# Kernel tuning notes

Measured on AMD Instinct MI355X. Metric: run time of the kernel, lower is better.

## Reference

```python
import jax, jax.numpy as jnp
import numpy as np

N_NODES = 50000
N_EDGES = 800000
IN_FEATS = 256
H_FEATS = 256
NUM_CLASSES = 128


def setup_inputs() -> dict:
    key = jax.random.key(0)
    ks = jax.random.split(key, 5)
    x = jax.random.normal(ks[0], (N_NODES, IN_FEATS), dtype=jnp.float32)
    src = jax.random.randint(ks[1], (N_EDGES,), 0, N_NODES, dtype=jnp.int64)
    dst = jax.random.randint(ks[2], (N_EDGES,), 0, N_NODES, dtype=jnp.int64)
    W1 = jax.random.normal(ks[3], (IN_FEATS, H_FEATS), dtype=jnp.float32) * (1.0 / np.sqrt(IN_FEATS))
    b1 = jnp.zeros((H_FEATS,), dtype=jnp.float32)
    W2 = jax.random.normal(ks[4], (H_FEATS, NUM_CLASSES), dtype=jnp.float32) * (1.0 / np.sqrt(H_FEATS))
    b2 = jnp.zeros((NUM_CLASSES,), dtype=jnp.float32)
    return {"x": x, "src": src, "dst": dst, "W1": W1, "b1": b1, "W2": W2, "b2": b2}


def _graph_conv(x, src, dst, norm_src, norm_dst, W, b):
    # DGL GraphConv, norm='both': D_out^{-1/2} A D_in^{-1/2} X W + b
    # project first (in_feats >= out_feats -> cheaper messages), math identical
    h = (x * norm_src[:, None]) @ W                      # [N, out]
    agg = jax.ops.segment_sum(h[src], dst, num_segments=N_NODES)  # gather + scatter-add
    return agg * norm_dst[:, None] + b


def reference(x, src, dst, W1, b1, W2, b2):
    ones = jnp.ones((N_EDGES,), dtype=x.dtype)
    deg_out = jax.ops.segment_sum(ones, src, num_segments=N_NODES)
    deg_in = jax.ops.segment_sum(ones, dst, num_segments=N_NODES)
    norm_src = jnp.clip(deg_out, 1.0, None) ** -0.5
    norm_dst = jnp.clip(deg_in, 1.0, None) ** -0.5

    h = _graph_conv(x, src, dst, norm_src, norm_dst, W1, b1)
    h = jax.nn.relu(h)
    out = _graph_conv(h, src, dst, norm_src, norm_dst, W2, b2)
    return out
```

## Files before the change

### kernel.cpp

```cpp
#include <hip/hip_runtime.h>

#define NNODES 50000
#define MPAD   50048
#define NEDGES 800000
#define KDIM   256
#define FH     256
#define FOUT   128

#define SHIFT  8
#define NBUCK  196
#define NB1    200
#define EPB    4000
#define CELLS  (NBUCK * NB1)
#define NSCAN  (2 * CELLS)
#define SCANB  ((NSCAN + 511) / 512)

typedef __bf16 bf16x8 __attribute__((ext_vector_type(8)));
typedef float floatx4 __attribute__((ext_vector_type(4)));

__device__ __forceinline__ float bf2f(unsigned short u) {
    union { unsigned int i; float f; } v;
    v.i = ((unsigned int)u) << 16;
    return v.f;
}
__device__ __forceinline__ unsigned short f2bf(float f) {
    union { float f; unsigned int i; } v;
    v.f = f;
    unsigned int r = v.i + 0x7FFFu + ((v.i >> 16) & 1u);
    return (unsigned short)(r >> 16);
}

__global__ __launch_bounds__(256) void l1_count_cast(const int* __restrict__ src,
                                                     const int* __restrict__ dst,
                                                     int* __restrict__ cell,
                                                     const float* __restrict__ W1,
                                                     unsigned short* __restrict__ Wt1,
                                                     const float* __restrict__ W2,
                                                     unsigned short* __restrict__ Wt2) {
    __shared__ int histD[256], histS[256];
    __shared__ float tile[32][33];
    const int tid = threadIdx.x;

    if (blockIdx.x >= NB1) {
        int b = blockIdx.x - NB1;
        const float* W; unsigned short* Wt; int N;
        if (b < 64) { W = W1; Wt = Wt1; N = FH; }
        else        { b -= 64; W = W2; Wt = Wt2; N = FOUT; }
        int kt = (b & 7) * 32;
        int nt = (b >> 3) * 32;
        int tx = tid & 31;
        int ty = tid >> 5;
        for (int r = ty; r < 32; r += 8)
            tile[r][tx] = W[(size_t)(kt + r) * N + nt + tx];
        __syncthreads();
        for (int r = ty; r < 32; r += 8)
            Wt[(size_t)(nt + r) * KDIM + kt + tx] = f2bf(tile[tx][r]);
        return;
    }

    const int b = blockIdx.x;
    const int base = b * EPB;
    histD[tid] = 0; histS[tid] = 0;
    __syncthreads();
    for (int g = tid; g < EPB / 4; g += 256) {
        uint4 s4 = *(const uint4*)(src + base + g * 4);
        uint4 d4 = *(const uint4*)(dst + base + g * 4);
        atomicAdd(&histD[d4.x >> SHIFT], 1);
        atomicAdd(&histD[d4.y >> SHIFT], 1);
        atomicAdd(&histD[d4.z >> SHIFT], 1);
        atomicAdd(&histD[d4.w >> SHIFT], 1);
        atomicAdd(&histS[s4.x >> SHIFT], 1);
        atomicAdd(&histS[s4.y >> SHIFT], 1);
        atomicAdd(&histS[s4.z >> SHIFT], 1);
        atomicAdd(&histS[s4.w >> SHIFT], 1);
    }
    __syncthreads();
    if (tid < NBUCK) {
        cell[tid * NB1 + b] = histD[tid];
        cell[CELLS + tid * NB1 + b] = histS[tid];
    }
}

__global__ __launch_bounds__(512) void scanA(int* __restrict__ data,
                                             int* __restrict__ sums, int n) {
    __shared__ int s[512];
    int tid = threadIdx.x;
    int i = blockIdx.x * 512 + tid;
    int v = (i < n) ? data[i] : 0;
    s[tid] = v;
    __syncthreads();
    for (int off = 1; off < 512; off <<= 1) {
        int t = (tid >= off) ? s[tid - off] : 0;
        __syncthreads();
        s[tid] += t;
        __syncthreads();
    }
    if (i < n) data[i] = s[tid] - v;
    if (tid == 511) sums[blockIdx.x] = s[511];
}

__global__ __launch_bounds__(512) void scanB(int* __restrict__ sums, int nb) {
    __shared__ int s[512];
    int tid = threadIdx.x;
    int v = (tid < nb) ? sums[tid] : 0;
    s[tid] = v;
    __syncthreads();
    for (int off = 1; off < 512; off <<= 1) {
        int t = (tid >= off) ? s[tid - off] : 0;
        __syncthreads();
        s[tid] += t;
        __syncthreads();
    }
    if (tid < nb) sums[tid] = s[tid] - v;
}

__global__ __launch_bounds__(512) void scanC(int* __restrict__ data,
                                             const int* __restrict__ sums, int n) {
    int i = blockIdx.x * 512 + threadIdx.x;
    if (i < n) data[i] += sums[blockIdx.x];
}

__global__ __launch_bounds__(256) void l1_scatter(const int* __restrict__ src,
                                                  const int* __restrict__ dst,
                                                  const int* __restrict__ cell,
                                                  unsigned int* __restrict__ tmp1,
                                                  unsigned char* __restrict__ tmp2) {
    __shared__ int histD[256], histS[256];
    __shared__ int exD[256], exS[256];
    __shared__ unsigned int bufD[EPB];
    __shared__ unsigned short bufS[EPB];
    const int b = blockIdx.x, tid = threadIdx.x;
    const int base = b * EPB;

    histD[tid] = 0; histS[tid] = 0;
    __syncthreads();
    for (int g = tid; g < EPB / 4; g += 256) {
        uint4 s4 = *(const uint4*)(src + base + g * 4);
        uint4 d4 = *(const uint4*)(dst + base + g * 4);
        atomicAdd(&histD[d4.x >> SHIFT], 1);
        atomicAdd(&histD[d4.y >> SHIFT], 1);
        atomicAdd(&histD[d4.z >> SHIFT], 1);
        atomicAdd(&histD[d4.w >> SHIFT], 1);
        atomicAdd(&histS[s4.x >> SHIFT], 1);
        atomicAdd(&histS[s4.y >> SHIFT], 1);
        atomicAdd(&histS[s4.z >> SHIFT], 1);
        atomicAdd(&histS[s4.w >> SHIFT], 1);
    }
    __syncthreads();
    int vD = histD[tid], vS = histS[tid];
    exD[tid] = vD; exS[tid] = vS;
    __syncthreads();
    for (int off = 1; off < 256; off <<= 1) {
        int tD = (tid >= off) ? exD[tid - off] : 0;
        int tS = (tid >= off) ? exS[tid - off] : 0;
        __syncthreads();
        exD[tid] += tD; exS[tid] += tS;
        __syncthreads();
    }
    int eD = exD[tid] - vD, eS = exS[tid] - vS;
    __syncthreads();
    exD[tid] = eD; exS[tid] = eS;
    histD[tid] = eD; histS[tid] = eS;
    __syncthreads();
    for (int g = tid; g < EPB / 4; g += 256) {
        uint4 s4 = *(const uint4*)(src + base + g * 4);
        uint4 d4 = *(const uint4*)(dst + base + g * 4);
        unsigned int ss[4] = {s4.x, s4.y, s4.z, s4.w};
        unsigned int dd[4] = {d4.x, d4.y, d4.z, d4.w};
#pragma unroll
        for (int j = 0; j < 4; ++j) {
            int p = atomicAdd(&histD[dd[j] >> SHIFT], 1);
            bufD[p] = (ss[j] << 16) | dd[j];
            int q = atomicAdd(&histS[ss[j] >> SHIFT], 1);
            bufS[q] = (unsigned short)ss[j];
        }
    }
    __syncthreads();
    for (int e = tid; e < EPB; e += 256) {
        unsigned int p = bufD[e];
        int k = (p & 0xFFFFu) >> SHIFT;
        tmp1[cell[k * NB1 + b] + (e - exD[k])] = p;
    }
    for (int e = tid; e < EPB; e += 256) {
        unsigned int s = bufS[e];
        int k = s >> SHIFT;
        tmp2[(cell[CELLS + k * NB1 + b] - NEDGES) + (e - exS[k])] = (unsigned char)(s & 255u);
    }
}

__global__ __launch_bounds__(256) void l2_both(const unsigned int* __restrict__ tmp1,
                                               const unsigned char* __restrict__ tmp2,
                                               const int* __restrict__ cell,
                                               int* __restrict__ row_ptr,
                                               float* __restrict__ norm_dst,
                                               float* __restrict__ norm_src,
                                               int* __restrict__ csr_src) {
    __shared__ int cnt[256], ofs[256], cur[256];
    const int tid = threadIdx.x;

    if (blockIdx.x >= NBUCK) {
        const int k = blockIdx.x - NBUCK;
        const int start = cell[CELLS + k * NB1] - NEDGES;
        const int end = (k + 1 < NBUCK) ? cell[CELLS + (k + 1) * NB1] - NEDGES : NEDGES;
        cnt[tid] = 0;
        __syncthreads();
        for (int e = start + tid; e < end; e += 256)
            atomicAdd(&cnt[tmp2[e]], 1);
        __syncthreads();
        int node = k * 256 + tid;
        if (node < NNODES) {
            int d = cnt[tid] < 1 ? 1 : cnt[tid];
            norm_src[node] = 1.0f / sqrtf((float)d);
        }
        return;
    }

    const int k = blockIdx.x;
    const int start = cell[k * NB1];
    const int end = (k + 1 < NBUCK) ? cell[(k + 1) * NB1] : NEDGES;
    cnt[tid] = 0;
    __syncthreads();
    for (int e = start + tid; e < end; e += 256)
        atomicAdd(&cnt[tmp1[e] & 255u], 1);
    __syncthreads();
    int v = cnt[tid];
    ofs[tid] = v;
    __syncthreads();
    for (int off = 1; off < 256; off <<= 1) {
        int t = (tid >= off) ? ofs[tid - off] : 0;
        __syncthreads();
        ofs[tid] += t;
        __syncthreads();
    }
    int excl = ofs[tid] - v;
    int node = k * 256 + tid;
    if (node < NNODES) {
        row_ptr[node] = start + excl;
        int d = v < 1 ? 1 : v;
        norm_dst[node] = 1.0f / sqrtf((float)d);
    }
    cur[tid] = start + excl;
    if (k == 0 && tid == 0) row_ptr[NNODES] = NEDGES;
    __syncthreads();
    for (int e = start + tid; e < end; e += 256) {
        unsigned int p = tmp1[e];
        int pos = atomicAdd(&cur[p & 255u], 1);
        csr_src[pos] = (int)(p >> 16);
    }
}


struct arawF { float4 v[8]; float sc; };
struct arawU { uint4 v[4]; };
template <typename TA> struct rawsel;
template <> struct rawsel<float> { using type = arawF; };
template <> struct rawsel<unsigned short> { using type = arawU; };

__device__ __forceinline__ void loadA_raw(const float* A, const float* norm,
                                          int mt, int arow, int akseg, arawF& r) {
    int row = mt * 64 + arow;
    if (row < NNODES) {
        const float* p = A + (size_t)row * KDIM + akseg;
#pragma unroll
        for (int j = 0; j < 8; ++j) r.v[j] = *(const float4*)(p + j * 4);
        r.sc = norm[row];
    } else {
        float4 z = {0.f, 0.f, 0.f, 0.f};
#pragma unroll
        for (int j = 0; j < 8; ++j) r.v[j] = z;
        r.sc = 0.f;
    }
}
__device__ __forceinline__ void loadA_raw(const unsigned short* A, const float*,
                                          int mt, int arow, int akseg, arawU& r) {
    const unsigned short* p = A + (size_t)(mt * 64 + arow) * KDIM + akseg;
#pragma unroll
    for (int j = 0; j < 4; ++j) r.v[j] = *(const uint4*)(p + j * 8);
}
__device__ __forceinline__ void writeA_lds(char* Asb, int arow, int akseg, const arawF& r) {
    const int s = (arow & 7) << 4;
    const int base = arow * 512;
#pragma unroll
    for (int j = 0; j < 4; ++j) {
        union { uint4 u; unsigned short h[8]; } o;
        float4 a = r.v[2 * j], b = r.v[2 * j + 1];
        o.h[0] = f2bf(a.x * r.sc); o.h[1] = f2bf(a.y * r.sc);
        o.h[2] = f2bf(a.z * r.sc); o.h[3] = f2bf(a.w * r.sc);
        o.h[4] = f2bf(b.x * r.sc); o.h[5] = f2bf(b.y * r.sc);
        o.h[6] = f2bf(b.z * r.sc); o.h[7] = f2bf(b.w * r.sc);
        *(uint4*)(Asb + base + (((akseg + j * 8) * 2) ^ s)) = o.u;
    }
}
__device__ __forceinline__ void writeA_lds(char* Asb, int arow, int akseg, const arawU& r) {
    const int s = (arow & 7) << 4;
    const int base = arow * 512;
#pragma unroll
    for (int j = 0; j < 4; ++j)
        *(uint4*)(Asb + base + (((akseg + j * 8) * 2) ^ s)) = r.v[j];
}

template <typename TA, bool SCALE, int NPANEL>
__global__ __launch_bounds__(512) void gemm_bres(const TA* __restrict__ A,
                                                 const unsigned short* __restrict__ Bt,
                                                 const float* __restrict__ norm,
                                                 unsigned short* __restrict__ C) {
    constexpr int N = 128 * NPANEL;
    constexpr int NTILES = MPAD / 64;
    __shared__ __align__(16) unsigned short Bs[128 * 256];
    __shared__ __align__(16) unsigned short As[64 * 256];
    char* Bsb = (char*)Bs;
    char* Asb = (char*)As;

    const int tid = threadIdx.x;
    const int lane = tid & 63;
    const int wave = tid >> 6;

    int col0, mt0, mstep;
    if (NPANEL == 2) {
        col0 = ((blockIdx.x >> 3) & 1) * 128;
        mt0 = ((blockIdx.x >> 4) << 3) + (blockIdx.x & 7);
        mstep = gridDim.x >> 1;
    } else {
        col0 = 0;
        mt0 = blockIdx.x;
        mstep = gridDim.x;
    }

    {
        int col = tid >> 2;
        int kq = (tid & 3) * 64;
        const unsigned short* bg = Bt + (size_t)(col0 + col) * KDIM + kq;
        const int s = (col & 7) << 4;
        const int base = col * 512;
#pragma unroll
        for (int j = 0; j < 8; ++j) {
            uint4 v = *(const uint4*)(bg + j * 8);
            *(uint4*)(Bsb + base + (((kq + j * 8) * 2) ^ s)) = v;
        }
    }

    const int arow = tid >> 3;
    const int akseg = (tid & 7) * 32;

    typename rawsel<TA>::type buf;
    loadA_raw(A, norm, mt0, arow, akseg, buf);
    writeA_lds(Asb, arow, akseg, buf);
    __syncthreads();
    int mt = mt0, mtn = mt0 + mstep;
    if (mtn < NTILES) loadA_raw(A, norm, mtn, arow, akseg, buf);

    const int wn = wave & 3, wm = wave >> 2;
    const int ar = lane & 15;
    const int fkb = (lane >> 4) << 4;
    const int rA0 = wm * 32 + ar,  rA1 = rA0 + 16;
    const int cB0 = wn * 32 + ar,  cB1 = cB0 + 16;
    const int aO0 = rA0 * 512, aS0 = (rA0 & 7) << 4;
    const int aO1 = rA1 * 512, aS1 = (rA1 & 7) << 4;
    const int bO0 = cB0 * 512, bS0 = (cB0 & 7) << 4;
    const int bO1 = cB1 * 512, bS1 = (cB1 & 7) << 4;
    const int rb = (lane >> 4) << 2, cc = lane & 15;

    for (;;) {
        floatx4 a00 = {}, a01 = {}, a10 = {}, a11 = {};
#pragma unroll
        for (int kk = 0; kk < 8; ++kk) {
            const int kb = kk * 64 + fkb;
            bf16x8 fa0 = *(const bf16x8*)(Asb + aO0 + (kb ^ aS0));
            bf16x8 fa1 = *(const bf16x8*)(Asb + aO1 + (kb ^ aS1));
            bf16x8 fb0 = *(const bf16x8*)(Bsb + bO0 + (kb ^ bS0));
            bf16x8 fb1 = *(const bf16x8*)(Bsb + bO1 + (kb ^ bS1));
            a00 = __builtin_amdgcn_mfma_f32_16x16x32_bf16(fa0, fb0, a00, 0, 0, 0);
            a01 = __builtin_amdgcn_mfma_f32_16x16x32_bf16(fa0, fb1, a01, 0, 0, 0);
            a10 = __builtin_amdgcn_mfma_f32_16x16x32_bf16(fa1, fb0, a10, 0, 0, 0);
            a11 = __builtin_amdgcn_mfma_f32_16x16x32_bf16(fa1, fb1, a11, 0, 0, 0);
        }
        {
            const int mBase = mt * 64 + wm * 32 + rb;
            const int cBase = col0 + wn * 32 + cc;
#pragma unroll
            for (int r = 0; r < 4; ++r) {
                int m = mBase + r;
                if (m < NNODES) {
                    C[(size_t)m * N + cBase]      = f2bf(a00[r]);
                    C[(size_t)m * N + cBase + 16] = f2bf(a01[r]);
                }
                int m2 = m + 16;
                if (m2 < NNODES) {
                    C[(size_t)m2 * N + cBase]      = f2bf(a10[r]);
                    C[(size_t)m2 * N + cBase + 16] = f2bf(a11[r]);
                }
            }
        }
        if (mtn >= NTILES) break;
        __syncthreads();
        writeA_lds(Asb, arow, akseg, buf);
        mt = mtn; mtn += mstep;
        __syncthreads();
        if (mtn < NTILES) loadA_raw(A, norm, mtn, arow, akseg, buf);
    }
}

__global__ __launch_bounds__(256) void agg1_kernel(const unsigned short* __restrict__ H,
                                                   const int* __restrict__ row_ptr,
                                                   const int* __restrict__ csr_src,
                                                   const float* __restrict__ norm_dst,
                                                   const float* __restrict__ norm_src,
                                                   const float* __restrict__ bias,
                                                   unsigned short* __restrict__ out) {
    const int F = 256;
    int node = blockIdx.x * 4 + (threadIdx.x >> 6);
    int lane = threadIdx.x & 63;
    int f0 = lane * 4;
    if (node >= NNODES) {
        if (node < MPAD) {
            ushort4 z = {0, 0, 0, 0};
            *(ushort4*)(out + (size_t)node * F + f0) = z;
        }
        return;
    }
    int e0 = row_ptr[node];
    int e1 = row_ptr[node + 1];

    float acc0 = 0.f, acc1 = 0.f, acc2 = 0.f, acc3 = 0.f;
    const unsigned short* Hl = H + f0;

    int e = e0;
    for (; e + 7 < e1; e += 8) {
        ushort4 v[8];
#pragma unroll
        for (int u = 0; u < 8; ++u)
            v[u] = *(const ushort4*)(Hl + (size_t)csr_src[e + u] * F);
#pragma unroll
        for (int u = 0; u < 8; ++u) {
            acc0 += bf2f(v[u].x); acc1 += bf2f(v[u].y);
            acc2 += bf2f(v[u].z); acc3 += bf2f(v[u].w);
        }
    }
    for (; e + 3 < e1; e += 4) {
        ushort4 v[4];
#pragma unroll
        for (int u = 0; u < 4; ++u)
            v[u] = *(const ushort4*)(Hl + (size_t)csr_src[e + u] * F);
#pragma unroll
        for (int u = 0; u < 4; ++u) {
            acc0 += bf2f(v[u].x); acc1 += bf2f(v[u].y);
            acc2 += bf2f(v[u].z); acc3 += bf2f(v[u].w);
        }
    }
    for (; e < e1; ++e) {
        ushort4 v = *(const ushort4*)(Hl + (size_t)csr_src[e] * F);
        acc0 += bf2f(v.x); acc1 += bf2f(v.y); acc2 += bf2f(v.z); acc3 += bf2f(v.w);
    }

    float nd = norm_dst[node];
    float ns = norm_src[node];
    float o0 = fmaxf(fmaf(acc0, nd, bias[f0 + 0]), 0.0f) * ns;
    float o1 = fmaxf(fmaf(acc1, nd, bias[f0 + 1]), 0.0f) * ns;
    float o2 = fmaxf(fmaf(acc2, nd, bias[f0 + 2]), 0.0f) * ns;
    float o3 = fmaxf(fmaf(acc3, nd, bias[f0 + 3]), 0.0f) * ns;
    ushort4 o;
    o.x = f2bf(o0); o.y = f2bf(o1); o.z = f2bf(o2); o.w = f2bf(o3);
    *(ushort4*)(out + (size_t)node * F + f0) = o;
}

__global__ __launch_bounds__(256) void agg2_kernel(const unsigned short* __restrict__ H,
                                                   const int* __restrict__ row_ptr,
                                                   const int* __restrict__ csr_src,
                                                   const float* __restrict__ norm_dst,
                                                   const float* __restrict__ bias,
                                                   float* __restrict__ out) {
    const int F = 128;
    int node = blockIdx.x * 8 + (threadIdx.x >> 5);
    if (node >= NNODES) return;
    int lane = threadIdx.x & 31;
    int f0 = lane * 4;
    int e0 = row_ptr[node];
    int e1 = row_ptr[node + 1];

    float acc0 = 0.f, acc1 = 0.f, acc2 = 0.f, acc3 = 0.f;
    const unsigned short* Hl = H + f0;

    int e = e0;
    for (; e + 7 < e1; e += 8) {
        ushort4 v[8];
#pragma unroll
        for (int u = 0; u < 8; ++u)
            v[u] = *(const ushort4*)(Hl + (size_t)csr_src[e + u] * F);
#pragma unroll
        for (int u = 0; u < 8; ++u) {
            acc0 += bf2f(v[u].x); acc1 += bf2f(v[u].y);
            acc2 += bf2f(v[u].z); acc3 += bf2f(v[u].w);
        }
    }
    for (; e + 3 < e1; e += 4) {
        ushort4 v[4];
#pragma unroll
        for (int u = 0; u < 4; ++u)
            v[u] = *(const ushort4*)(Hl + (size_t)csr_src[e + u] * F);
#pragma unroll
        for (int u = 0; u < 4; ++u) {
            acc0 += bf2f(v[u].x); acc1 += bf2f(v[u].y);
            acc2 += bf2f(v[u].z); acc3 += bf2f(v[u].w);
        }
    }
    for (; e < e1; ++e) {
        ushort4 v = *(const ushort4*)(Hl + (size_t)csr_src[e] * F);
        acc0 += bf2f(v.x); acc1 += bf2f(v.y); acc2 += bf2f(v.z); acc3 += bf2f(v.w);
    }

    float nd = norm_dst[node];
    float4 o;
    o.x = fmaf(acc0, nd, bias[f0 + 0]);
    o.y = fmaf(acc1, nd, bias[f0 + 1]);
    o.z = fmaf(acc2, nd, bias[f0 + 2]);
    o.w = fmaf(acc3, nd, bias[f0 + 3]);
    *(float4*)(out + (size_t)node * F + f0) = o;
}

extern "C" void kernel_launch(void* const* d_in, const int* in_sizes, int n_in,
                              void* d_out, int out_size, void* d_ws, size_t ws_size,
                              hipStream_t stream) {
    const float* x   = (const float*)d_in[0];
    const int*   src = (const int*)d_in[1];
    const int*   dst = (const int*)d_in[2];
    const float* W1  = (const float*)d_in[3];
    const float* b1  = (const float*)d_in[4];
    const float* W2  = (const float*)d_in[5];
    const float* b2  = (const float*)d_in[6];
    float* out = (float*)d_out;

    char* ws = (char*)d_ws;
    size_t off = 0;
    auto alloc = [&](size_t bytes) {
        char* p = ws + off;
        off += (bytes + 255) & ~(size_t)255;
        return p;
    };
    float* norm_src  = (float*)alloc(NNODES * 4);
    float* norm_dst  = (float*)alloc(NNODES * 4);
    int*   cell      = (int*)alloc((size_t)NSCAN * 4);
    int*   ssum      = (int*)alloc(512 * 4);
    unsigned int*  tmp1 = (unsigned int*)alloc((size_t)NEDGES * 4);
    unsigned char* tmp2 = (unsigned char*)alloc((size_t)NEDGES);
    int*   row_ptr   = (int*)alloc((NNODES + 16) * 4);
    int*   csr_src   = (int*)alloc(NEDGES * 4);
    unsigned short* h   = (unsigned short*)alloc((size_t)MPAD * FH * 2);
    unsigned short* h1  = (unsigned short*)alloc((size_t)MPAD * FH * 2);
    unsigned short* Wt1 = (unsigned short*)alloc((size_t)FH * KDIM * 2);
    unsigned short* Wt2 = (unsigned short*)alloc((size_t)FOUT * KDIM * 2);
    unsigned short* h2  = h;

    l1_count_cast<<<NB1 + 96, 256, 0, stream>>>(src, dst, cell, W1, Wt1, W2, Wt2);
    scanA<<<SCANB, 512, 0, stream>>>(cell, ssum, NSCAN);
    scanB<<<1, 512, 0, stream>>>(ssum, SCANB);
    scanC<<<SCANB, 512, 0, stream>>>(cell, ssum, NSCAN);
    l1_scatter<<<NB1, 256, 0, stream>>>(src, dst, cell, tmp1, tmp2);
    l2_both<<<2 * NBUCK, 256, 0, stream>>>(tmp1, tmp2, cell, row_ptr, norm_dst, norm_src, csr_src);

    gemm_bres<float, true, 2><<<512, 512, 0, stream>>>(x, Wt1, norm_src, h);
    agg1_kernel<<<MPAD / 4, 256, 0, stream>>>(h, row_ptr, csr_src, norm_dst, norm_src, b1, h1);

    gemm_bres<unsigned short, false, 1><<<256, 512, 0, stream>>>(h1, Wt2, nullptr, h2);
    agg2_kernel<<<(NNODES + 7) / 8, 256, 0, stream>>>(h2, row_ptr, csr_src, norm_dst, b2, out);
}
```

Before: 268.5 us.

## Drop global scan for block-local sort; widen aggregation gathers to 16-byte lanes

Merges the count and scatter passes into one kernel that sorts each block's edges locally and stores per-block exclusive offsets, which removes the three scan kernels and the second edge read. The CSR build kernel now reads per-block segments serially with one thread per segment and reduces the offsets to find the bucket base. Both aggregation kernels are rewritten so each lane loads 8 bf16 values (uint4) and several nodes share a wavefront, with padding rows used for inactive edges. The GEMM drops its row bound checks and writes padded rows. The serial per-thread segment loops in l2_both may be slow, and padded-row reads rely on the zeroed padding of h and h2 being valid.

```diff
diff --git a/kernel.cpp b/kernel.cpp
--- a/kernel.cpp
+++ b/kernel.cpp
@@ -11,9 +11,6 @@
 #define NBUCK  196
 #define NB1    200
 #define EPB    4000
-#define CELLS  (NBUCK * NB1)
-#define NSCAN  (2 * CELLS)
-#define SCANB  ((NSCAN + 511) / 512)
 
 typedef __bf16 bf16x8 __attribute__((ext_vector_type(8)));
 typedef float floatx4 __attribute__((ext_vector_type(4)));
@@ -30,14 +27,19 @@
     return (unsigned short)(r >> 16);
 }
 
-__global__ __launch_bounds__(256) void l1_count_cast(const int* __restrict__ src,
-                                                     const int* __restrict__ dst,
-                                                     int* __restrict__ cell,
-                                                     const float* __restrict__ W1,
-                                                     unsigned short* __restrict__ Wt1,
-                                                     const float* __restrict__ W2,
-                                                     unsigned short* __restrict__ Wt2) {
-    __shared__ int histD[256], histS[256];
+__global__ __launch_bounds__(256) void l1_sort_cast(const int* __restrict__ src,
+                                                    const int* __restrict__ dst,
+                                                    unsigned int* __restrict__ tmp1,
+                                                    unsigned char* __restrict__ tmp2,
+                                                    int* __restrict__ exD_arr,
+                                                    int* __restrict__ exS_arr,
+                                                    const float* __restrict__ W1,
+                                                    unsigned short* __restrict__ Wt1,
+                                                    const float* __restrict__ W2,
+                                                    unsigned short* __restrict__ Wt2) {
+    __shared__ int histD[256], histS[256], exD[256], exS[256];
+    __shared__ unsigned int bufD[EPB];
+    __shared__ unsigned short bufS[EPB];
     __shared__ float tile[32][33];
     const int tid = threadIdx.x;
 
@@ -75,78 +77,6 @@
         atomicAdd(&histS[s4.w >> SHIFT], 1);
     }
     __syncthreads();
-    if (tid < NBUCK) {
-        cell[tid * NB1 + b] = histD[tid];
-        cell[CELLS + tid * NB1 + b] = histS[tid];
-    }
-}
-
-__global__ __launch_bounds__(512) void scanA(int* __restrict__ data,
-                                             int* __restrict__ sums, int n) {
-    __shared__ int s[512];
-    int tid = threadIdx.x;
-    int i = blockIdx.x * 512 + tid;
-    int v = (i < n) ? data[i] : 0;
-    s[tid] = v;
-    __syncthreads();
-    for (int off = 1; off < 512; off <<= 1) {
-        int t = (tid >= off) ? s[tid - off] : 0;
-        __syncthreads();
-        s[tid] += t;
-        __syncthreads();
-    }
-    if (i < n) data[i] = s[tid] - v;
-    if (tid == 511) sums[blockIdx.x] = s[511];
-}
-
-__global__ __launch_bounds__(512) void scanB(int* __restrict__ sums, int nb) {
-    __shared__ int s[512];
-    int tid = threadIdx.x;
-    int v = (tid < nb) ? sums[tid] : 0;
-    s[tid] = v;
-    __syncthreads();
-    for (int off = 1; off < 512; off <<= 1) {
-        int t = (tid >= off) ? s[tid - off] : 0;
-        __syncthreads();
-        s[tid] += t;
-        __syncthreads();
-    }
-    if (tid < nb) sums[tid] = s[tid] - v;
-}
-
-__global__ __launch_bounds__(512) void scanC(int* __restrict__ data,
-                                             const int* __restrict__ sums, int n) {
-    int i = blockIdx.x * 512 + threadIdx.x;
-    if (i < n) data[i] += sums[blockIdx.x];
-}
-
-__global__ __launch_bounds__(256) void l1_scatter(const int* __restrict__ src,
-                                                  const int* __restrict__ dst,
-                                                  const int* __restrict__ cell,
-                                                  unsigned int* __restrict__ tmp1,
-                                                  unsigned char* __restrict__ tmp2) {
-    __shared__ int histD[256], histS[256];
-    __shared__ int exD[256], exS[256];
-    __shared__ unsigned int bufD[EPB];
-    __shared__ unsigned short bufS[EPB];
-    const int b = blockIdx.x, tid = threadIdx.x;
-    const int base = b * EPB;
-
-    histD[tid] = 0; histS[tid] = 0;
-    __syncthreads();
-    for (int g = tid; g < EPB / 4; g += 256) {
-        uint4 s4 = *(const uint4*)(src + base + g * 4);
-        uint4 d4 = *(const uint4*)(dst + base + g * 4);
-        atomicAdd(&histD[d4.x >> SHIFT], 1);
-        atomicAdd(&histD[d4.y >> SHIFT], 1);
-        atomicAdd(&histD[d4.z >> SHIFT], 1);
-        atomicAdd(&histD[d4.w >> SHIFT], 1);
-        atomicAdd(&histS[s4.x >> SHIFT], 1);
-        atomicAdd(&histS[s4.y >> SHIFT], 1);
-        atomicAdd(&histS[s4.z >> SHIFT], 1);
-        atomicAdd(&histS[s4.w >> SHIFT], 1);
-    }
-    __syncthreads();
     int vD = histD[tid], vS = histS[tid];
     exD[tid] = vD; exS[tid] = vS;
     __syncthreads();
@@ -158,8 +88,9 @@
         __syncthreads();
     }
     int eD = exD[tid] - vD, eS = exS[tid] - vS;
-    __syncthreads();
-    exD[tid] = eD; exS[tid] = eS;
+    exD_arr[tid * NB1 + b] = eD;
+    exS_arr[tid * NB1 + b] = eS;
+    __syncthreads();
     histD[tid] = eD; histS[tid] = eS;
     __syncthreads();
     for (int g = tid; g < EPB / 4; g += 256) {
@@ -176,36 +107,36 @@
         }
     }
     __syncthreads();
-    for (int e = tid; e < EPB; e += 256) {
-        unsigned int p = bufD[e];
-        int k = (p & 0xFFFFu) >> SHIFT;
-        tmp1[cell[k * NB1 + b] + (e - exD[k])] = p;
-    }
-    for (int e = tid; e < EPB; e += 256) {
-        unsigned int s = bufS[e];
-        int k = s >> SHIFT;
-        tmp2[(cell[CELLS + k * NB1 + b] - NEDGES) + (e - exS[k])] = (unsigned char)(s & 255u);
-    }
+    for (int e = tid; e < EPB; e += 256) tmp1[base + e] = bufD[e];
+    for (int e = tid; e < EPB; e += 256) tmp2[base + e] = (unsigned char)(bufS[e] & 255u);
 }
 
 __global__ __launch_bounds__(256) void l2_both(const unsigned int* __restrict__ tmp1,
                                                const unsigned char* __restrict__ tmp2,
-                                               const int* __restrict__ cell,
+                                               const int* __restrict__ exD_arr,
+                                               const int* __restrict__ exS_arr,
                                                int* __restrict__ row_ptr,
                                                float* __restrict__ norm_dst,
                                                float* __restrict__ norm_src,
                                                int* __restrict__ csr_src) {
-    __shared__ int cnt[256], ofs[256], cur[256];
+    __shared__ int cnt[256], ofs[256], cur[256], red[256];
+    __shared__ int segoff[NB1], seglen[NB1];
     const int tid = threadIdx.x;
 
     if (blockIdx.x >= NBUCK) {
         const int k = blockIdx.x - NBUCK;
-        const int start = cell[CELLS + k * NB1] - NEDGES;
-        const int end = (k + 1 < NBUCK) ? cell[CELLS + (k + 1) * NB1] - NEDGES : NEDGES;
+        if (tid < NB1) {
+            int e0 = exS_arr[k * NB1 + tid];
+            segoff[tid] = tid * EPB + e0;
+            seglen[tid] = exS_arr[(k + 1) * NB1 + tid] - e0;
+        }
         cnt[tid] = 0;
         __syncthreads();
-        for (int e = start + tid; e < end; e += 256)
-            atomicAdd(&cnt[tmp2[e]], 1);
+        if (tid < NB1) {
+            int so = segoff[tid], sl = seglen[tid];
+            for (int i = 0; i < sl; ++i)
+                atomicAdd(&cnt[tmp2[so + i]], 1);
+        }
         __syncthreads();
         int node = k * 256 + tid;
         if (node < NNODES) {
@@ -216,12 +147,25 @@
     }
 
     const int k = blockIdx.x;
-    const int start = cell[k * NB1];
-    const int end = (k + 1 < NBUCK) ? cell[(k + 1) * NB1] : NEDGES;
+    int e0v = 0;
+    if (tid < NB1) {
+        e0v = exD_arr[k * NB1 + tid];
+        segoff[tid] = tid * EPB + e0v;
+        seglen[tid] = exD_arr[(k + 1) * NB1 + tid] - e0v;
+    }
+    red[tid] = (tid < NB1) ? e0v : 0;
     cnt[tid] = 0;
     __syncthreads();
-    for (int e = start + tid; e < end; e += 256)
-        atomicAdd(&cnt[tmp1[e] & 255u], 1);
+    for (int off = 128; off > 0; off >>= 1) {
+        if (tid < off) red[tid] += red[tid + off];
+        __syncthreads();
+    }
+    const int base = red[0];
+    if (tid < NB1) {
+        int so = segoff[tid], sl = seglen[tid];
+        for (int i = 0; i < sl; ++i)
+            atomicAdd(&cnt[tmp1[so + i] & 255u], 1);
+    }
     __syncthreads();
     int v = cnt[tid];
     ofs[tid] = v;
@@ -235,20 +179,22 @@
     int excl = ofs[tid] - v;
     int node = k * 256 + tid;
     if (node < NNODES) {
-        row_ptr[node] = start + excl;
+        row_ptr[node] = base + excl;
         int d = v < 1 ? 1 : v;
         norm_dst[node] = 1.0f / sqrtf((float)d);
     }
-    cur[tid] = start + excl;
+    cur[tid] = base + excl;
     if (k == 0 && tid == 0) row_ptr[NNODES] = NEDGES;
     __syncthreads();
-    for (int e = start + tid; e < end; e += 256) {
-        unsigned int p = tmp1[e];
-        int pos = atomicAdd(&cur[p & 255u], 1);
-        csr_src[pos] = (int)(p >> 16);
-    }
-}
-
+    if (tid < NB1) {
+        int so = segoff[tid], sl = seglen[tid];
+        for (int i = 0; i < sl; ++i) {
+            unsigned int p = tmp1[so + i];
+            int pos = atomicAdd(&cur[p & 255u], 1);
+            csr_src[pos] = (int)(p >> 16);
+        }
+    }
+}
 
 struct arawF { float4 v[8]; float sc; };
 struct arawU { uint4 v[4]; };
@@ -380,15 +326,11 @@
 #pragma unroll
             for (int r = 0; r < 4; ++r) {
                 int m = mBase + r;
-                if (m < NNODES) {
-                    C[(size_t)m * N + cBase]      = f2bf(a00[r]);
-                    C[(size_t)m * N + cBase + 16] = f2bf(a01[r]);
-                }
+                C[(size_t)m * N + cBase]      = f2bf(a00[r]);
+                C[(size_t)m * N + cBase + 16] = f2bf(a01[r]);
                 int m2 = m + 16;
-                if (m2 < NNODES) {
-                    C[(size_t)m2 * N + cBase]      = f2bf(a10[r]);
-                    C[(size_t)m2 * N + cBase + 16] = f2bf(a11[r]);
-                }
+                C[(size_t)m2 * N + cBase]      = f2bf(a10[r]);
+                C[(size_t)m2 * N + cBase + 16] = f2bf(a11[r]);
             }
         }
         if (mtn >= NTILES) break;
@@ -408,59 +350,54 @@
                                                    const float* __restrict__ bias,
                                                    unsigned short* __restrict__ out) {
     const int F = 256;
-    int node = blockIdx.x * 4 + (threadIdx.x >> 6);
-    int lane = threadIdx.x & 63;
-    int f0 = lane * 4;
-    if (node >= NNODES) {
-        if (node < MPAD) {
-            ushort4 z = {0, 0, 0, 0};
-            *(ushort4*)(out + (size_t)node * F + f0) = z;
-        }
-        return;
-    }
-    int e0 = row_ptr[node];
-    int e1 = row_ptr[node + 1];
-
-    float acc0 = 0.f, acc1 = 0.f, acc2 = 0.f, acc3 = 0.f;
+    const int tid = threadIdx.x;
+    const int lane = tid & 63;
+    const int half = lane >> 5;
+    const int f0 = (lane & 31) * 8;
+    const int nA = __builtin_amdgcn_readfirstlane(blockIdx.x * 8 + (tid >> 6) * 2);
+    const int node = nA + half;
+
+    const int rp0 = row_ptr[nA < NNODES ? nA : NNODES];
+    const int rp1 = row_ptr[nA + 1 < NNODES ? nA + 1 : NNODES];
+    const int rp2 = row_ptr[nA + 2 < NNODES ? nA + 2 : NNODES];
+    const int degA = rp1 - rp0, degB = rp2 - rp1;
+    const int nIter = degA > degB ? degA : degB;
+
     const unsigned short* Hl = H + f0;
-
-    int e = e0;
-    for (; e + 7 < e1; e += 8) {
-        ushort4 v[8];
-#pragma unroll
-        for (int u = 0; u < 8; ++u)
-            v[u] = *(const ushort4*)(Hl + (size_t)csr_src[e + u] * F);
-#pragma unroll
-        for (int u = 0; u < 8; ++u) {
-            acc0 += bf2f(v[u].x); acc1 += bf2f(v[u].y);
-            acc2 += bf2f(v[u].z); acc3 += bf2f(v[u].w);
-        }
-    }
-    for (; e + 3 < e1; e += 4) {
-        ushort4 v[4];
+    float acc[8] = {};
+
+    for (int it = 0; it < nIter; it += 4) {
+        int ix[4];
+#pragma unroll
+        for (int u = 0; u < 4; ++u) {
+            int iA = csr_src[rp0 + it + u];
+            int iB = csr_src[rp1 + it + u];
+            iA = (it + u < degA) ? iA : NNODES;
+            iB = (it + u < degB) ? iB : NNODES;
+            ix[u] = half ? iB : iA;
+        }
+        uint4 v[4];
 #pragma unroll
         for (int u = 0; u < 4; ++u)
-            v[u] = *(const ushort4*)(Hl + (size_t)csr_src[e + u] * F);
+            v[u] = *(const uint4*)(Hl + (size_t)ix[u] * F);
 #pragma unroll
         for (int u = 0; u < 4; ++u) {
-            acc0 += bf2f(v[u].x); acc1 += bf2f(v[u].y);
-            acc2 += bf2f(v[u].z); acc3 += bf2f(v[u].w);
-        }
-    }
-    for (; e < e1; ++e) {
-        ushort4 v = *(const ushort4*)(Hl + (size_t)csr_src[e] * F);
-        acc0 += bf2f(v.x); acc1 += bf2f(v.y); acc2 += bf2f(v.z); acc3 += bf2f(v.w);
-    }
-
-    float nd = norm_dst[node];
-    float ns = norm_src[node];
-    float o0 = fmaxf(fmaf(acc0, nd, bias[f0 + 0]), 0.0f) * ns;
-    float o1 = fmaxf(fmaf(acc1, nd, bias[f0 + 1]), 0.0f) * ns;
-    float o2 = fmaxf(fmaf(acc2, nd, bias[f0 + 2]), 0.0f) * ns;
-    float o3 = fmaxf(fmaf(acc3, nd, bias[f0 + 3]), 0.0f) * ns;
-    ushort4 o;
-    o.x = f2bf(o0); o.y = f2bf(o1); o.z = f2bf(o2); o.w = f2bf(o3);
-    *(ushort4*)(out + (size_t)node * F + f0) = o;
+            const unsigned short* pv = (const unsigned short*)&v[u];
+#pragma unroll
+            for (int j = 0; j < 8; ++j) acc[j] += bf2f(pv[j]);
+        }
+    }
+
+    float nd = 0.f, ns = 0.f;
+    if (node < NNODES) { nd = norm_dst[node]; ns = norm_src[node]; }
+    float4 b0 = *(const float4*)(bias + f0);
+    float4 b1v = *(const float4*)(bias + f0 + 4);
+    float bb[8] = {b0.x, b0.y, b0.z, b0.w, b1v.x, b1v.y, b1v.z, b1v.w};
+    union { uint4 u; unsigned short s[8]; } o;
+#pragma unroll
+    for (int j = 0; j < 8; ++j)
+        o.s[j] = f2bf(fmaxf(fmaf(acc[j], nd, bb[j]), 0.f) * ns);
+    *(uint4*)(out + (size_t)node * F + f0) = o.u;
 }
 
 __global__ __launch_bounds__(256) void agg2_kernel(const unsigned short* __restrict__ H,
@@ -470,51 +407,66 @@
                                                    const float* __restrict__ bias,
                                                    float* __restrict__ out) {
     const int F = 128;
-    int node = blockIdx.x * 8 + (threadIdx.x >> 5);
-    if (node >= NNODES) return;
-    int lane = threadIdx.x & 31;
-    int f0 = lane * 4;
-    int e0 = row_ptr[node];
-    int e1 = row_ptr[node + 1];
-
-    float acc0 = 0.f, acc1 = 0.f, acc2 = 0.f, acc3 = 0.f;
+    const int tid = threadIdx.x;
+    const int lane = tid & 63;
+    const int q = lane >> 4;
+    const int f0 = (lane & 15) * 8;
+    const int n0 = __builtin_amdgcn_readfirstlane(blockIdx.x * 16 + (tid >> 6) * 4);
+    const int node = n0 + q;
+
+    int rp[5];
+#pragma unroll
+    for (int j = 0; j < 5; ++j) rp[j] = row_ptr[(n0 + j) < NNODES ? (n0 + j) : NNODES];
+    int dg[4];
+    int nIter = 0;
+#pragma unroll
+    for (int j = 0; j < 4; ++j) { dg[j] = rp[j + 1] - rp[j]; nIter = dg[j] > nIter ? dg[j] : nIter; }
+
     const unsigned short* Hl = H + f0;
-
-    int e = e0;
-    for (; e + 7 < e1; e += 8) {
-        ushort4 v[8];
-#pragma unroll
-        for (int u = 0; u < 8; ++u)
-            v[u] = *(const ushort4*)(Hl + (size_t)csr_src[e + u] * F);
-#pragma unroll
-        for (int u = 0; u < 8; ++u) {
-            acc0 += bf2f(v[u].x); acc1 += bf2f(v[u].y);
-            acc2 += bf2f(v[u].z); acc3 += bf2f(v[u].w);
-        }
-    }
-    for (; e + 3 < e1; e += 4) {
-        ushort4 v[4];
+    float acc[8] = {};
+
+    for (int it = 0; it < nIter; it += 4) {
+        int ix[4];
+#pragma unroll
+        for (int u = 0; u < 4; ++u) {
+            int i0 = csr_src[rp[0] + it + u];
+            int i1 = csr_src[rp[1] + it + u];
+            int i2 = csr_src[rp[2] + it + u];
+            int i3 = csr_src[rp[3] + it + u];
+            i0 = (it + u < dg[0]) ? i0 : NNODES;
+            i1 = (it + u < dg[1]) ? i1 : NNODES;
+            i2 = (it + u < dg[2]) ? i2 : NNODES;
+            i3 = (it + u < dg[3]) ? i3 : NNODES;
+            int ilo = (q & 1) ? i1 : i0;
+            int ihi = (q & 1) ? i3 : i2;
+            ix[u] = (q & 2) ? ihi : ilo;
+        }
+        uint4 v[4];
 #pragma unroll
         for (int u = 0; u < 4; ++u)
-            v[u] = *(const ushort4*)(Hl + (size_t)csr_src[e + u] * F);
+            v[u] = *(const uint4*)(Hl + (size_t)ix[u] * F);
 #pragma unroll
         for (int u = 0; u < 4; ++u) {
-            acc0 += bf2f(v[u].x); acc1 += bf2f(v[u].y);
-            acc2 += bf2f(v[u].z); acc3 += bf2f(v[u].w);
-        }
-    }
-    for (; e < e1; ++e) {
-        ushort4 v = *(const ushort4*)(Hl + (size_t)csr_src[e] * F);
-        acc0 += bf2f(v.x); acc1 += bf2f(v.y); acc2 += bf2f(v.z); acc3 += bf2f(v.w);
-    }
-
-    float nd = norm_dst[node];
-    float4 o;
-    o.x = fmaf(acc0, nd, bias[f0 + 0]);
-    o.y = fmaf(acc1, nd, bias[f0 + 1]);
-    o.z = fmaf(acc2, nd, bias[f0 + 2]);
-    o.w = fmaf(acc3, nd, bias[f0 + 3]);
-    *(float4*)(out + (size_t)node * F + f0) = o;
+            const unsigned short* pv = (const unsigned short*)&v[u];
+#pragma unroll
+            for (int j = 0; j < 8; ++j) acc[j] += bf2f(pv[j]);
+        }
+    }
+
+    if (node < NNODES) {
+        float nd = norm_dst[node];
+        float4 o1, o2;
+        o1.x = fmaf(acc[0], nd, bias[f0 + 0]);
+        o1.y = fmaf(acc[1], nd, bias[f0 + 1]);
+        o1.z = fmaf(acc[2], nd, bias[f0 + 2]);
+        o1.w = fmaf(acc[3], nd, bias[f0 + 3]);
+        o2.x = fmaf(acc[4], nd, bias[f0 + 4]);
+        o2.y = fmaf(acc[5], nd, bias[f0 + 5]);
+        o2.z = fmaf(acc[6], nd, bias[f0 + 6]);
+        o2.w = fmaf(acc[7], nd, bias[f0 + 7]);
+        *(float4*)(out + (size_t)node * F + f0) = o1;
+        *(float4*)(out + (size_t)node * F + f0 + 4) = o2;
+    }
 }
 
 extern "C" void kernel_launch(void* const* d_in, const int* in_sizes, int n_in,
@@ -538,28 +490,26 @@
     };
     float* norm_src  = (float*)alloc(NNODES * 4);
     float* norm_dst  = (float*)alloc(NNODES * 4);
-    int*   cell      = (int*)alloc((size_t)NSCAN * 4);
-    int*   ssum      = (int*)alloc(512 * 4);
+    int*   exD_arr   = (int*)alloc((size_t)256 * NB1 * 4);
+    int*   exS_arr   = (int*)alloc((size_t)256 * NB1 * 4);
     unsigned int*  tmp1 = (unsigned int*)alloc((size_t)NEDGES * 4);
     unsigned char* tmp2 = (unsigned char*)alloc((size_t)NEDGES);
     int*   row_ptr   = (int*)alloc((NNODES + 16) * 4);
-    int*   csr_src   = (int*)alloc(NEDGES * 4);
+    int*   csr_src   = (int*)alloc((size_t)(NEDGES + 256) * 4);
     unsigned short* h   = (unsigned short*)alloc((size_t)MPAD * FH * 2);
     unsigned short* h1  = (unsigned short*)alloc((size_t)MPAD * FH * 2);
     unsigned short* Wt1 = (unsigned short*)alloc((size_t)FH * KDIM * 2);
     unsigned short* Wt2 = (unsigned short*)alloc((size_t)FOUT * KDIM * 2);
     unsigned short* h2  = h;
 
-    l1_count_cast<<<NB1 + 96, 256, 0, stream>>>(src, dst, cell, W1, Wt1, W2, Wt2);
-    scanA<<<SCANB, 512, 0, stream>>>(cell, ssum, NSCAN);
-    scanB<<<1, 512, 0, stream>>>(ssum, SCANB);
-    scanC<<<SCANB, 512, 0, stream>>>(cell, ssum, NSCAN);
-    l1_scatter<<<NB1, 256, 0, stream>>>(src, dst, cell, tmp1, tmp2);
-    l2_both<<<2 * NBUCK, 256, 0, stream>>>(tmp1, tmp2, cell, row_ptr, norm_dst, norm_src, csr_src);
+    l1_sort_cast<<<NB1 + 96, 256, 0, stream>>>(src, dst, tmp1, tmp2, exD_arr, exS_arr,
+                                               W1, Wt1, W2, Wt2);
+    l2_both<<<2 * NBUCK, 256, 0, stream>>>(tmp1, tmp2, exD_arr, exS_arr,
+                                           row_ptr, norm_dst, norm_src, csr_src);
 
     gemm_bres<float, true, 2><<<512, 512, 0, stream>>>(x, Wt1, norm_src, h);
-    agg1_kernel<<<MPAD / 4, 256, 0, stream>>>(h, row_ptr, csr_src, norm_dst, norm_src, b1, h1);
+    agg1_kernel<<<MPAD / 8, 256, 0, stream>>>(h, row_ptr, csr_src, norm_dst, norm_src, b1, h1);
 
     gemm_bres<unsigned short, false, 1><<<256, 512, 0, stream>>>(h1, Wt2, nullptr, h2);
-    agg2_kernel<<<(NNODES + 7) / 8, 256, 0, stream>>>(h2, row_ptr, csr_src, norm_dst, b2, out);
-}
+    agg2_kernel<<<(NNODES + 15) / 16, 256, 0, stream>>>(h2, row_ptr, csr_src, norm_dst, b2, out);
+}
```

New measurement: 252.7 us. 1.06x faster.
